# Kernel tuning notes

Measured on AMD Instinct MI355X. Metric: run time of the kernel, lower is better.

The kernel has to match this reference:

```python
import jax, jax.numpy as jnp
import numpy as np

B, N, F, T = 64, 1024, 8, 12
H, NLAYERS, K, OUT = 32, 3, 10, 12
E_RAND = N * 32


def setup_inputs() -> dict:
    key = jax.random.key(0)
    ks = jax.random.split(key, 11)
    x = jax.random.normal(ks[0], (B, N, F, T), jnp.float32)
    src = jax.random.randint(ks[1], (E_RAND,), 0, N)
    dst = jax.random.randint(ks[2], (E_RAND,), 0, N)
    loop = jnp.arange(N)
    edge_index = jnp.stack([jnp.concatenate([src, loop]),
                            jnp.concatenate([dst, loop])]).astype(jnp.int32)
    # weights in (0.1, 1.0) so all degrees are strictly positive
    edge_weight = jax.random.uniform(ks[3], (E_RAND + N,), jnp.float32, 0.1, 1.0)
    s = 0.1  # ~ 1/sqrt(H) init scale, matches torch defaults in spirit
    gru_w_ih = jax.random.normal(ks[4], (3 * H, F), jnp.float32) * s
    gru_w_hh = jax.random.normal(ks[5], (3 * H, H), jnp.float32) * s
    gru_b_ih = jax.random.normal(ks[6], (3 * H,), jnp.float32) * s
    gru_b_hh = jax.random.normal(ks[7], (3 * H,), jnp.float32) * s
    conv_w = jax.random.normal(ks[8], (NLAYERS, H, H), jnp.float32) * (1.0 / np.sqrt(H))
    lin_w = jax.random.normal(ks[9], (H, OUT), jnp.float32) * (1.0 / np.sqrt(H))
    lin_b = jax.random.normal(ks[10], (OUT,), jnp.float32) * s
    return {"x": x, "edge_index": edge_index, "edge_weight": edge_weight,
            "gru_w_ih": gru_w_ih, "gru_w_hh": gru_w_hh,
            "gru_b_ih": gru_b_ih, "gru_b_hh": gru_b_hh,
            "conv_w": conv_w, "lin_w": lin_w, "lin_b": lin_b}


def reference(x, edge_index, edge_weight, gru_w_ih, gru_w_hh, gru_b_ih, gru_b_hh,
              conv_w, lin_w, lin_b):
    Bsz, Nn, Fe, Tt = x.shape
    Hh = gru_w_hh.shape[1]

    # ---- temporal GRU over [B*N, T, F], keep last hidden state ----
    xt = jnp.transpose(x, (0, 1, 3, 2)).reshape(Bsz * Nn, Tt, Fe)
    gates_x = xt @ gru_w_ih.T + gru_b_ih  # [BN, T, 3H], input gates precomputed

    def step(h, gx):
        gh = h @ gru_w_hh.T + gru_b_hh
        xr, xz, xn = jnp.split(gx, 3, axis=-1)
        hr, hz, hn = jnp.split(gh, 3, axis=-1)
        r = jax.nn.sigmoid(xr + hr)
        z = jax.nn.sigmoid(xz + hz)
        n = jnp.tanh(xn + r * hn)
        return (1.0 - z) * n + z * h, None

    h0 = jnp.zeros((Bsz * Nn, Hh), x.dtype)
    hT, _ = jax.lax.scan(step, h0, jnp.swapaxes(gates_x, 0, 1))
    h = hT.reshape(Bsz, Nn, Hh)  # [B, N, H]

    # ---- normalized Laplacian (shared across batch) ----
    A = jnp.zeros((Nn, Nn), x.dtype).at[edge_index[0], edge_index[1]].add(edge_weight)
    d_isqrt = 1.0 / jnp.sqrt(A.sum(axis=1))  # row-degree, matches A.sum(dim=2)
    Lap = jnp.eye(Nn, dtype=x.dtype) - d_isqrt[:, None] * A * d_isqrt[None, :]

    # ---- rank-K spectral filter: M = U_k diag(S_k) U_k^T ----
    # torch code SVDs the identical L[b] per batch element; sign flips of U
    # columns cancel in U_k (.) U_k^T, so one SVD is mathematically identical.
    U, S, _ = jnp.linalg.svd(Lap, full_matrices=False)
    M = (U[:, :K] * S[:K]) @ U[:, :K].T  # [N, N]

    for w in conv_w:  # static 3-layer loop
        h = jax.nn.relu(jnp.einsum('nm,bmh,hk->bnk', M, h, w)) + h

    return h @ lin_w + lin_b  # [B, N, 12]
```

## Files before the change

kernel.cpp:

```cpp
#include <hip/hip_runtime.h>
#include <math.h>


#define NN 1024
#define PP 48
#define JSWEEPS 3
#define NROUNDS (JSWEEPS * (PP - 1))

typedef float v2f __attribute__((ext_vector_type(2)));

__global__ __launch_bounds__(256) void k_gru(
    const float* __restrict__ x, const float* __restrict__ wih,
    const float* __restrict__ whh, const float* __restrict__ bih,
    const float* __restrict__ bhh, float* __restrict__ hout) {
  __shared__ float s_x[64][97];
  __shared__ float s_h[64][33];
  int tid = threadIdx.x;
  int row = tid & 63;
  int i_base = __builtin_amdgcn_readfirstlane((tid >> 6) * 8);
  long row0 = (long)blockIdx.x * 64;

  for (int i = tid; i < 64 * 24; i += 256) {
    int r = i / 24, c = i % 24;
    float4 v = *(const float4*)&x[(row0 + r) * 96 + c * 4];
    s_x[r][c * 4 + 0] = v.x; s_x[r][c * 4 + 1] = v.y;
    s_x[r][c * 4 + 2] = v.z; s_x[r][c * 4 + 3] = v.w;
  }
  for (int i = tid; i < 64 * 32; i += 256) s_h[i / 32][i % 32] = 0.f;
  __syncthreads();

  v2f h2[16];
#pragma unroll
  for (int k2 = 0; k2 < 16; ++k2) h2[k2] = (v2f){0.f, 0.f};

  for (int t = 0; t < 12; ++t) {
    v2f x2[4];
#pragma unroll
    for (int f2 = 0; f2 < 4; ++f2)
      x2[f2] = (v2f){s_x[row][(2 * f2) * 12 + t], s_x[row][(2 * f2 + 1) * 12 + t]};
    for (int ii = 0; ii < 8; ++ii) {
      int i = i_base + ii;
      const v2f* wr = (const v2f*)(wih + i * 8);
      const v2f* wz = (const v2f*)(wih + (32 + i) * 8);
      const v2f* wn = (const v2f*)(wih + (64 + i) * 8);
      const v2f* hr = (const v2f*)(whh + i * 32);
      const v2f* hz = (const v2f*)(whh + (32 + i) * 32);
      const v2f* hn = (const v2f*)(whh + (64 + i) * 32);
      v2f ar2 = (v2f){0.f, 0.f}, az2 = (v2f){0.f, 0.f};
      v2f gx2 = (v2f){0.f, 0.f}, gh2 = (v2f){0.f, 0.f};
#pragma unroll
      for (int f2 = 0; f2 < 4; ++f2) {
        ar2 += x2[f2] * wr[f2];
        az2 += x2[f2] * wz[f2];
        gx2 += x2[f2] * wn[f2];
      }
#pragma unroll
      for (int k2 = 0; k2 < 16; ++k2) {
        ar2 += h2[k2] * hr[k2];
        az2 += h2[k2] * hz[k2];
        gh2 += h2[k2] * hn[k2];
      }
      float ar = ar2.x + ar2.y + bih[i] + bhh[i];
      float az = az2.x + az2.y + bih[32 + i] + bhh[32 + i];
      float gx = gx2.x + gx2.y + bih[64 + i];
      float gh = gh2.x + gh2.y + bhh[64 + i];
      ar = fminf(fmaxf(ar, -30.f), 30.f);
      az = fminf(fmaxf(az, -30.f), 30.f);
      float r = __frcp_rn(1.f + __expf(-ar));
      float z = __frcp_rn(1.f + __expf(-az));
      float a = gx + r * gh;
      a = fminf(fmaxf(a, -15.f), 15.f);
      float e2 = __expf(2.f * a);
      float n = (e2 - 1.f) * __frcp_rn(e2 + 1.f);
      float hold = s_h[row][i];
      s_h[row][i] = (1.f - z) * n + z * hold;
    }
    __syncthreads();
#pragma unroll
    for (int k2 = 0; k2 < 16; ++k2)
      h2[k2] = (v2f){s_h[row][2 * k2], s_h[row][2 * k2 + 1]};
    __syncthreads();
  }
  for (int idx = tid; idx < 64 * 8; idx += 256) {
    int r = idx >> 3, c4 = idx & 7;
    float4 v = make_float4(s_h[r][c4 * 4], s_h[r][c4 * 4 + 1],
                           s_h[r][c4 * 4 + 2], s_h[r][c4 * 4 + 3]);
    *(float4*)&hout[(row0 + r) * 32 + c4 * 4] = v;
  }
}

__global__ void k_scatter(const int* __restrict__ ei, const float* __restrict__ ew,
                          float* __restrict__ A, int E) {
  int e = blockIdx.x * 256 + threadIdx.x;
  if (e < E) atomicAdd(&A[ei[e] * NN + ei[E + e]], ew[e]);
}

__global__ __launch_bounds__(256) void k_degree(const float* __restrict__ A,
                                                float* __restrict__ disq) {
  __shared__ float red[256];
  int row = blockIdx.x, tid = threadIdx.x;
  float s = 0.f;
  for (int j = tid; j < NN; j += 256) s += A[row * NN + j];
  red[tid] = s;
  __syncthreads();
  for (int off = 128; off > 0; off >>= 1) {
    if (tid < off) red[tid] += red[tid + off];
    __syncthreads();
  }
  if (tid == 0) disq[row] = 1.f / sqrtf(red[0]);
}

template <int LAP>
__global__ __launch_bounds__(256) void k_mmsplit(const float* __restrict__ A,
                                                 const float* __restrict__ disq,
                                                 float* __restrict__ Cp) {
  __shared__ float As[32][68];
  __shared__ float Bs[32][68];
  int tid = threadIdx.x;
  int tx = tid & 15, ty = tid >> 4;
  int i0 = blockIdx.y * 64, j0 = blockIdx.x * 64;
  int kbase = blockIdx.z * 512;
  v2f acc2[4][2];
#pragma unroll
  for (int a = 0; a < 4; ++a) {
    acc2[a][0] = (v2f){0.f, 0.f};
    acc2[a][1] = (v2f){0.f, 0.f};
  }
  int lrow = tid >> 3;
  int kk0 = (tid & 7) * 4;
  float drA0 = 0.f, drA1 = 0.f, drB0 = 0.f, drB1 = 0.f;
  if (LAP) {
    drA0 = disq[i0 + lrow]; drA1 = disq[i0 + lrow + 32];
    drB0 = disq[j0 + lrow]; drB1 = disq[j0 + lrow + 32];
  }
  float4 pa0 = *(const float4*)&A[(long)(i0 + lrow) * NN + kbase + kk0];
  float4 pa1 = *(const float4*)&A[(long)(i0 + lrow + 32) * NN + kbase + kk0];
  float4 pb0 = *(const float4*)&A[(long)(j0 + lrow) * NN + kbase + kk0];
  float4 pb1 = *(const float4*)&A[(long)(j0 + lrow + 32) * NN + kbase + kk0];
  for (int k0 = kbase; k0 < kbase + 512; k0 += 32) {
    if (LAP) {
      float4 dq = *(const float4*)&disq[k0 + kk0];
      int kg = k0 + kk0;
#pragma unroll
      for (int e = 0; e < 4; ++e) {
        float dqe = (e == 0) ? dq.x : (e == 1) ? dq.y : (e == 2) ? dq.z : dq.w;
        float a0e = (e == 0) ? pa0.x : (e == 1) ? pa0.y : (e == 2) ? pa0.z : pa0.w;
        float a1e = (e == 0) ? pa1.x : (e == 1) ? pa1.y : (e == 2) ? pa1.z : pa1.w;
        float b0e = (e == 0) ? pb0.x : (e == 1) ? pb0.y : (e == 2) ? pb0.z : pb0.w;
        float b1e = (e == 0) ? pb1.x : (e == 1) ? pb1.y : (e == 2) ? pb1.z : pb1.w;
        As[kk0 + e][lrow]      = -drA0 * a0e * dqe + ((i0 + lrow == kg + e) ? 1.f : 0.f);
        As[kk0 + e][lrow + 32] = -drA1 * a1e * dqe + ((i0 + lrow + 32 == kg + e) ? 1.f : 0.f);
        Bs[kk0 + e][lrow]      = -drB0 * b0e * dqe + ((j0 + lrow == kg + e) ? 1.f : 0.f);
        Bs[kk0 + e][lrow + 32] = -drB1 * b1e * dqe + ((j0 + lrow + 32 == kg + e) ? 1.f : 0.f);
      }
    } else {
      As[kk0 + 0][lrow] = pa0.x; As[kk0 + 1][lrow] = pa0.y;
      As[kk0 + 2][lrow] = pa0.z; As[kk0 + 3][lrow] = pa0.w;
      As[kk0 + 0][lrow + 32] = pa1.x; As[kk0 + 1][lrow + 32] = pa1.y;
      As[kk0 + 2][lrow + 32] = pa1.z; As[kk0 + 3][lrow + 32] = pa1.w;
      Bs[kk0 + 0][lrow] = pb0.x; Bs[kk0 + 1][lrow] = pb0.y;
      Bs[kk0 + 2][lrow] = pb0.z; Bs[kk0 + 3][lrow] = pb0.w;
      Bs[kk0 + 0][lrow + 32] = pb1.x; Bs[kk0 + 1][lrow + 32] = pb1.y;
      Bs[kk0 + 2][lrow + 32] = pb1.z; Bs[kk0 + 3][lrow + 32] = pb1.w;
    }
    __syncthreads();
    if (k0 + 32 < kbase + 512) {
      pa0 = *(const float4*)&A[(long)(i0 + lrow) * NN + k0 + 32 + kk0];
      pa1 = *(const float4*)&A[(long)(i0 + lrow + 32) * NN + k0 + 32 + kk0];
      pb0 = *(const float4*)&A[(long)(j0 + lrow) * NN + k0 + 32 + kk0];
      pb1 = *(const float4*)&A[(long)(j0 + lrow + 32) * NN + k0 + 32 + kk0];
    }
#pragma unroll
    for (int kk = 0; kk < 32; ++kk) {
      float4 av = *(const float4*)&As[kk][ty * 4];
      const v2f* bp = (const v2f*)&Bs[kk][tx * 4];
      v2f bv0 = bp[0], bv1 = bp[1];
      float aa[4] = {av.x, av.y, av.z, av.w};
#pragma unroll
      for (int a = 0; a < 4; ++a) {
        v2f ab = (v2f){aa[a], aa[a]};
        acc2[a][0] += ab * bv0;
        acc2[a][1] += ab * bv1;
      }
    }
    __syncthreads();
  }
  float* cp = Cp + (long)blockIdx.z * (NN * NN);
#pragma unroll
  for (int a = 0; a < 4; ++a) {
    float4 v = make_float4(acc2[a][0].x, acc2[a][0].y,
                           acc2[a][1].x, acc2[a][1].y);
    *(float4*)&cp[(long)(i0 + ty * 4 + a) * NN + j0 + tx * 4] = v;
  }
}

__global__ __launch_bounds__(256) void k_fold(const float* __restrict__ Cp,
                                              float* __restrict__ C) {
  int i = (blockIdx.x * 256 + threadIdx.x) * 4;
  float4 a = *(const float4*)&Cp[i];
  float4 b = *(const float4*)&Cp[i + NN * NN];
  float4 v = make_float4(a.x + b.x, a.y + b.y, a.z + b.z, a.w + b.w);
  *(float4*)&C[i] = v;
}

__global__ void k_q0(float* __restrict__ Q) {
  int i = blockIdx.x * 256 + threadIdx.x;
  if (i < NN * PP) {
    unsigned u = (unsigned)i * 2654435761u;
    u ^= u >> 16; u *= 2246822519u; u ^= u >> 13; u *= 3266489917u; u ^= u >> 16;
    Q[i] = (float)(u & 0xFFFFFF) * (1.f / 16777216.f) - 0.5f;
  }
}

__global__ __launch_bounds__(256) void k_spmm(const float* __restrict__ Gp,
                                              const float* __restrict__ Q,
                                              float* __restrict__ Zp) {
  __shared__ float Qs[64][49];
  __shared__ float Gs[16][65];
  int tid = threadIdx.x;
  int r = tid >> 4;
  int c0 = (tid & 15) * 3;
  int row0 = blockIdx.x * 16;
  int k0 = blockIdx.y * 256;
  float a0 = 0.f, a1 = 0.f, a2 = 0.f;
  for (int kt = 0; kt < 4; ++kt) {
    int kb = k0 + kt * 64;
    for (int idx = tid; idx < 64 * PP; idx += 256) {
      int qr = idx / PP, qc = idx % PP;
      Qs[qr][qc] = Q[(kb + qr) * PP + qc];
    }
    for (int idx = tid; idx < 16 * 64; idx += 256) {
      int gr = idx >> 6, gk = idx & 63;
      Gs[gr][gk] = Gp[(long)(row0 + gr) * NN + kb + gk];
    }
    __syncthreads();
#pragma unroll 4
    for (int kk = 0; kk < 64; ++kk) {
      float g = Gs[r][kk];
      a0 += g * Qs[kk][c0];
      a1 += g * Qs[kk][c0 + 1];
      a2 += g * Qs[kk][c0 + 2];
    }
    __syncthreads();
  }
  float* zp = Zp + (long)blockIdx.y * (NN * PP);
  zp[(row0 + r) * PP + c0] = a0;
  zp[(row0 + r) * PP + c0 + 1] = a1;
  zp[(row0 + r) * PP + c0 + 2] = a2;
}

__global__ __launch_bounds__(256) void k_gram(const float* __restrict__ Zp,
                                              float* __restrict__ Z,
                                              float* __restrict__ Sp) {
  __shared__ float Zs[32][49];
  int tid = threadIdx.x;
  int r0 = blockIdx.x * 32;
  for (int idx = tid; idx < 32 * PP; idx += 256) {
    int r = idx / PP, c = idx % PP;
    long g = (long)(r0 + r) * PP + c;
    float s = Zp[g] + Zp[g + NN * PP] + Zp[g + 2 * NN * PP] + Zp[g + 3 * NN * PP];
    Zs[r][c] = s;
    Z[g] = s;
  }
  __syncthreads();
  float* sp = Sp + blockIdx.x * (PP * PP);
  for (int cell = tid; cell < PP * PP; cell += 256) {
    int i = cell / PP, j = cell % PP;
    float a = 0.f;
#pragma unroll 8
    for (int r = 0; r < 32; ++r) a += Zs[r][i] * Zs[r][j];
    sp[cell] = a;
  }
}

__global__ __launch_bounds__(256) void k_tbuild(const float* __restrict__ Qa,
                                                const float* __restrict__ Zp,
                                                float* __restrict__ Tp) {
  __shared__ float Qs[32][49];
  __shared__ float Ys[32][49];
  int tid = threadIdx.x;
  int r0 = blockIdx.x * 32;
  for (int idx = tid; idx < 32 * PP; idx += 256) {
    int r = idx / PP, c = idx % PP;
    long g = (long)(r0 + r) * PP + c;
    Qs[r][c] = Qa[g];
    Ys[r][c] = Zp[g] + Zp[g + NN * PP] + Zp[g + 2 * NN * PP] + Zp[g + 3 * NN * PP];
  }
  __syncthreads();
  float* tp = Tp + blockIdx.x * (PP * PP);
  for (int cell = tid; cell < PP * PP; cell += 256) {
    int i = cell / PP, j = cell % PP;
    float a = 0.f;
#pragma unroll 8
    for (int r = 0; r < 32; ++r) a += Qs[r][i] * Ys[r][j];
    tp[cell] = a;
  }
}

__global__ __launch_bounds__(256) void k_qr(const float* __restrict__ Sp,
                                            float* __restrict__ Q) {
  __shared__ float R[PP][PP + 1];
  __shared__ float rs[PP];
  __shared__ float idiag[PP];
  int tid = threadIdx.x;
  for (int idx = tid; idx < PP * PP; idx += 256) {
    float s = 0.f;
    for (int b = 0; b < 32; ++b) s += Sp[b * (PP * PP) + idx];
    R[idx / PP][idx % PP] = s;
  }
  __syncthreads();
  for (int j = 0; j < PP; ++j) {
    float d = R[j][j];
    float sq = sqrtf(d > 1e-30f ? d : 1e-30f);
    float invd = 1.f / sq;
    for (int c = j + tid; c < PP; c += 256)
      rs[c] = (c == j) ? sq : R[j][c] * invd;
    __syncthreads();
    int m = PP - 1 - j;
    for (int idx = tid; idx < m * m; idx += 256) {
      int i = j + 1 + idx / m, c = j + 1 + idx % m;
      R[i][c] -= rs[i] * rs[c];
    }
    for (int c = j + tid; c < PP; c += 256) R[j][c] = rs[c];
    __syncthreads();
  }
  if (tid < PP) idiag[tid] = 1.f / R[tid][tid];
  __syncthreads();
  int row = blockIdx.x * 256 + tid;
  float q[PP];
#pragma unroll
  for (int k = 0; k < PP; ++k) q[k] = Q[row * PP + k];
#pragma unroll
  for (int c = 0; c < PP; ++c) {
    float s = q[c];
#pragma unroll
    for (int k = 0; k < c; ++k) s -= q[k] * R[k][c];
    q[c] = s * idiag[c];
  }
#pragma unroll
  for (int k = 0; k < PP; ++k) Q[row * PP + k] = q[k];
}

__global__ __launch_bounds__(448) void k_jacobi(const float* __restrict__ Tp,
                                                float* __restrict__ Vsel,
                                                float* __restrict__ s10) {
  __shared__ float Ta[PP][PP + 1], Tb[PP][PP + 1];
  __shared__ float Va[PP][PP + 1], Vb[PP][PP + 1];
  __shared__ float cw0[2][PP], cw1[2][PP];
  __shared__ int ci0[2][PP], ci1[2][PP];
  __shared__ int ppair[2][24], qpair[2][24];
  __shared__ float cpair[2][24], spair[2][24];
  __shared__ int selidx[10];
  int tid = threadIdx.x;
  for (int idx = tid; idx < PP * PP; idx += 448) {
    float s = 0.f;
    for (int b = 0; b < 32; ++b) s += Tp[b * (PP * PP) + idx];
    Tb[idx / PP][idx % PP] = s;
  }
  __syncthreads();
  for (int idx = tid; idx < PP * PP; idx += 448) {
    int i = idx / PP, j = idx % PP;
    Ta[i][j] = 0.5f * (Tb[i][j] + Tb[j][i]);
    Va[i][j] = (i == j) ? 1.f : 0.f;
  }
  if (tid < PP) {
    ci0[0][tid] = tid; ci1[0][tid] = tid;
    cw0[0][tid] = 1.f; cw1[0][tid] = 0.f;
  }
  __syncthreads();
  float (*Tc)[PP + 1] = Ta, (*Tn)[PP + 1] = Tb;
  float (*Vc)[PP + 1] = Va, (*Vn)[PP + 1] = Vb;

  auto coeff_phase = [&](int rr, int cur, int nxt, float (*Tcur)[PP + 1]) {
    int k = tid - 384;
    int P = (k == 0) ? 0 : ((rr + k - 1) % 47) + 1;
    int Q = ((rr + 46 - k) % 47) + 1;
    int P0 = ci0[cur][P], P1 = ci1[cur][P];
    float Pw0 = cw0[cur][P], Pw1 = cw1[cur][P];
    int Q0 = ci0[cur][Q], Q1 = ci1[cur][Q];
    float Qw0 = cw0[cur][Q], Qw1 = cw1[cur][Q];
    float app = Pw0 * (Pw0 * Tcur[P0][P0] + Pw1 * Tcur[P0][P1]) +
                Pw1 * (Pw0 * Tcur[P1][P0] + Pw1 * Tcur[P1][P1]);
    float apq = Pw0 * (Qw0 * Tcur[P0][Q0] + Qw1 * Tcur[P0][Q1]) +
                Pw1 * (Qw0 * Tcur[P1][Q0] + Qw1 * Tcur[P1][Q1]);
    float aqq = Qw0 * (Qw0 * Tcur[Q0][Q0] + Qw1 * Tcur[Q0][Q1]) +
                Qw1 * (Qw0 * Tcur[Q1][Q0] + Qw1 * Tcur[Q1][Q1]);
    float c = 1.f, s = 0.f;
    if (fabsf(apq) > 1e-30f) {
      float tau = (aqq - app) / (2.f * apq);
      float den = fabsf(tau) + sqrtf(1.f + tau * tau);
      float tt = copysignf(1.f / den, tau);
      c = 1.f / sqrtf(1.f + tt * tt);
      s = tt * c;
    }
    ci0[nxt][P] = P; ci1[nxt][P] = Q; cw0[nxt][P] = c;  cw1[nxt][P] = -s;
    ci0[nxt][Q] = P; ci1[nxt][Q] = Q; cw0[nxt][Q] = s;  cw1[nxt][Q] = c;
    ppair[nxt][k] = P; qpair[nxt][k] = Q;
    cpair[nxt][k] = c; spair[nxt][k] = s;
  };

  if (tid >= 384 && tid < 408) coeff_phase(0, 0, 1, Tc);
  __syncthreads();

  int cur = 1;
  int i_row = tid >> 3;
  int kb = (tid & 7) * 3;
  for (int R = 0; R < NROUNDS; ++R) {
    if (tid < 384) {
      float wi0 = cw0[cur][i_row], wi1 = cw1[cur][i_row];
      int i0 = ci0[cur][i_row], i1 = ci1[cur][i_row];
#pragma unroll
      for (int m = 0; m < 3; ++m) {
        int k = kb + m;
        int p = ppair[cur][k], q = qpair[cur][k];
        float c = cpair[cur][k], s = spair[cur][k];
        float t00 = Tc[i0][p], t01 = Tc[i0][q];
        float t10 = Tc[i1][p], t11 = Tc[i1][q];
        float rp = wi0 * t00 + wi1 * t10;
        float rq = wi0 * t01 + wi1 * t11;
        Tn[i_row][p] = c * rp - s * rq;
        Tn[i_row][q] = s * rp + c * rq;
        float v0 = Vc[i_row][p], v1 = Vc[i_row][q];
        Vn[i_row][p] = c * v0 - s * v1;
        Vn[i_row][q] = s * v0 + c * v1;
      }
    } else if (tid < 408 && R + 1 < NROUNDS) {
      coeff_phase((R + 1) % 47, cur, cur ^ 1, Tc);
    }
    __syncthreads();
    float (*tt_)[PP + 1] = Tc; Tc = Tn; Tn = tt_;
    float (*vt_)[PP + 1] = Vc; Vc = Vn; Vn = vt_;
    cur ^= 1;
  }

  if (tid < 64) {
    float v = (tid < PP) ? Tc[tid][tid] : -1e30f;
    for (int sel = 0; sel < 10; ++sel) {
      float bv = v; int bi = tid;
      for (int off = 32; off > 0; off >>= 1) {
        float ov = __shfl_xor(bv, off);
        int oi = __shfl_xor(bi, off);
        if (ov > bv || (ov == bv && oi < bi)) { bv = ov; bi = oi; }
      }
      if (tid == 0) { selidx[sel] = bi; s10[sel] = sqrtf(fmaxf(bv, 0.f)); }
      if (tid == bi) v = -1e30f;
    }
  }
  __syncthreads();
  for (int idx = tid; idx < PP * 10; idx += 448) {
    int j = idx / 10, i = idx % 10;
    Vsel[idx] = Vc[j][selidx[i]];
  }
}

__global__ __launch_bounds__(256) void k_u10(const float* __restrict__ Q,
                                             const float* __restrict__ Vsel,
                                             float* __restrict__ U10) {
  __shared__ float Vs[PP * 10];
  int tid = threadIdx.x;
  for (int idx = tid; idx < PP * 10; idx += 256) Vs[idx] = Vsel[idx];
  __syncthreads();
  int row = blockIdx.x * 256 + tid;
  float q[PP];
#pragma unroll
  for (int k = 0; k < PP; ++k) q[k] = Q[row * PP + k];
#pragma unroll
  for (int i = 0; i < 10; ++i) {
    float s = 0.f;
#pragma unroll
    for (int k = 0; k < PP; ++k) s += q[k] * Vs[k * 10 + i];
    U10[row * 10 + i] = s;
  }
}

__global__ __launch_bounds__(320) void k_p0(const float* __restrict__ h,
                                            const float* __restrict__ U10,
                                            float* __restrict__ Pp) {
  __shared__ float Hs[128][33];
  __shared__ float Us[128][10];
  int tid = threadIdx.x;
  int b = blockIdx.x >> 2, ch = blockIdx.x & 3;
  int i = tid / 32, kk = tid % 32;
  int base = ch * 256;
  v2f acc2 = (v2f){0.f, 0.f};
  for (int t0 = 0; t0 < 256; t0 += 128) {
    for (int idx = tid; idx < 128 * 32; idx += 320) {
      int r = idx / 32, c = idx % 32;
      Hs[r][c] = h[(long)(b * NN + base + t0 + r) * 32 + c];
    }
    for (int idx = tid; idx < 1280; idx += 320)
      Us[idx / 10][idx % 10] = U10[(base + t0 + idx / 10) * 10 + idx % 10];
    __syncthreads();
#pragma unroll 8
    for (int r = 0; r < 128; r += 2) {
      acc2 += (v2f){Us[r][i], Us[r + 1][i]} * (v2f){Hs[r][kk], Hs[r + 1][kk]};
    }
    __syncthreads();
  }
  Pp[(long)blockIdx.x * 320 + tid] = acc2.x + acc2.y;
}

template <int LAST>
__global__ __launch_bounds__(256) void k_update(float* __restrict__ h,
                                                const float* __restrict__ U10,
                                                const float* __restrict__ Pp,
                                                const float* __restrict__ W,
                                                const float* __restrict__ s10,
                                                const float* __restrict__ lw,
                                                const float* __restrict__ lb,
                                                float* __restrict__ out) {
  __shared__ float P0s[10][32];
  __shared__ float P1s[10][32];
  __shared__ float Ws[32][32];
  __shared__ float Us[64][10];
  __shared__ float hl[64][33];
  int tid = threadIdx.x;
  int b = blockIdx.x, n0 = blockIdx.y * 64;
  for (int idx = tid; idx < 320; idx += 256) {
    long g = (long)b * 4 * 320 + idx;
    P0s[idx / 32][idx % 32] = Pp[g] + Pp[g + 320] + Pp[g + 640] + Pp[g + 960];
  }
  for (int idx = tid; idx < 1024; idx += 256) Ws[idx / 32][idx % 32] = W[idx];
  for (int idx = tid; idx < 640; idx += 256)
    Us[idx / 10][idx % 10] = U10[(n0 + idx / 10) * 10 + idx % 10];
  __syncthreads();
  for (int idx = tid; idx < 320; idx += 256) {
    int i = idx / 32, kk = idx % 32;
    float a = 0.f;
#pragma unroll
    for (int j = 0; j < 32; ++j) a += P0s[i][j] * Ws[j][kk];
    P1s[i][kk] = s10[i] * a;
  }
  __syncthreads();
  for (int idx = tid; idx < 2048; idx += 256) {
    int nl = idx / 32, k = idx % 32;
    float z = 0.f;
#pragma unroll
    for (int i = 0; i < 10; ++i) z += Us[nl][i] * P1s[i][k];
    long g = (long)(b * NN + n0 + nl) * 32 + k;
    float hn = h[g] + fmaxf(z, 0.f);
    if (LAST) hl[nl][k] = hn;
    else h[g] = hn;
  }
  if (LAST) {
    __syncthreads();
    for (int idx = tid; idx < 64 * 12; idx += 256) {
      int row = idx / 12, o = idx % 12;
      float s = lb[o];
#pragma unroll
      for (int j = 0; j < 32; ++j) s += hl[row][j] * lw[j * 12 + o];
      out[(long)(b * NN + n0 + row) * 12 + o] = s;
    }
  }
}

extern "C" void kernel_launch(void* const* d_in, const int* in_sizes, int n_in,
                              void* d_out, int out_size, void* d_ws, size_t ws_size,
                              hipStream_t stream) {
  const float* x    = (const float*)d_in[0];
  const int*   ei   = (const int*)d_in[1];
  const float* ew   = (const float*)d_in[2];
  const float* wih  = (const float*)d_in[3];
  const float* whh  = (const float*)d_in[4];
  const float* bih  = (const float*)d_in[5];
  const float* bhh  = (const float*)d_in[6];
  const float* convw = (const float*)d_in[7];
  const float* lw   = (const float*)d_in[8];
  const float* lb   = (const float*)d_in[9];
  float* out = (float*)d_out;
  float* ws  = (float*)d_ws;
  int E = in_sizes[1] / 2;

  float* h    = ws;
  float* B1   = h + 2097152;
  float* B2   = B1 + 1048576;
  float* B3   = B2 + 1048576;
  float* Qa   = B3 + 1048576;
  float* Qb   = Qa + 49152;
  float* Zp   = Qb + 49152;
  float* Sp   = Zp + 196608;
  float* Tp   = Sp + 73728;
  float* Vsel = Tp + 73728;
  float* s10  = Vsel + 480;
  float* U10  = s10 + 16;
  float* disq = U10 + 10240;
  float* Pp   = Zp;
  float* Cp   = h;

  hipMemsetAsync(B1, 0, (size_t)1048576 * 4, stream);
  k_scatter<<<(E + 255) / 256, 256, 0, stream>>>(ei, ew, B1, E);
  k_degree<<<NN, 256, 0, stream>>>(B1, disq);
  k_mmsplit<1><<<dim3(16, 16, 2), 256, 0, stream>>>(B1, disq, Cp);
  k_fold<<<1024, 256, 0, stream>>>(Cp, B2);
  k_mmsplit<0><<<dim3(16, 16, 2), 256, 0, stream>>>(B2, disq, Cp);
  k_fold<<<1024, 256, 0, stream>>>(Cp, B3);
  k_mmsplit<0><<<dim3(16, 16, 2), 256, 0, stream>>>(B3, disq, Cp);
  k_fold<<<1024, 256, 0, stream>>>(Cp, B1);
  k_mmsplit<0><<<dim3(16, 16, 2), 256, 0, stream>>>(B1, disq, Cp);
  k_fold<<<1024, 256, 0, stream>>>(Cp, B3);
  k_mmsplit<0><<<dim3(16, 16, 2), 256, 0, stream>>>(B3, disq, Cp);
  k_fold<<<1024, 256, 0, stream>>>(Cp, B1);
  k_mmsplit<0><<<dim3(16, 16, 2), 256, 0, stream>>>(B1, disq, Cp);
  k_fold<<<1024, 256, 0, stream>>>(Cp, B3);

  k_q0<<<192, 256, 0, stream>>>(Qa);
  for (int it = 0; it < 6; ++it) {
    float* src = (it & 1) ? Qb : Qa;
    float* dst = (it & 1) ? Qa : Qb;
    k_spmm<<<dim3(64, 4), 256, 0, stream>>>(B3, src, Zp);
    k_gram<<<32, 256, 0, stream>>>(Zp, dst, Sp);
    k_qr<<<4, 256, 0, stream>>>(Sp, dst);
  }

  k_spmm<<<dim3(64, 4), 256, 0, stream>>>(B2, Qa, Zp);
  k_tbuild<<<32, 256, 0, stream>>>(Qa, Zp, Tp);
  k_jacobi<<<1, 448, 0, stream>>>(Tp, Vsel, s10);
  k_u10<<<4, 256, 0, stream>>>(Qa, Vsel, U10);

  k_gru<<<1024, 256, 0, stream>>>(x, wih, whh, bih, bhh, h);

  for (int l = 0; l < 3; ++l) {
    k_p0<<<256, 320, 0, stream>>>(h, U10, Pp);
    if (l < 2)
      k_update<0><<<dim3(64, 16), 256, 0, stream>>>(h, U10, Pp, convw + l * 1024,
                                                    s10, lw, lb, out);
    else
      k_update<1><<<dim3(64, 16), 256, 0, stream>>>(h, U10, Pp, convw + l * 1024,
                                                    s10, lw, lb, out);
  }
}
```

Before: 1.073 ms.

## Retile Gram-power matmuls to 128x128 blocks with 4-way split-K

Replaces the 64x64-tile, 2-way split-K matmul with a 128x128-tile kernel where each thread computes an 8x8 output block over 16-deep K slices, using 4-way split-K. The aim is higher register-level reuse and fewer LDS reads per FMA in the six repeated-squaring matmuls. To hold the extra partial sums, buffers are reassigned and a new B4 buffer is added, and the fold kernel now sums four partials instead of two. The cost is more fold traffic, higher register pressure and a larger workspace. Grid size drops from 512 to 256 blocks.

```diff
diff --git a/kernel.cpp b/kernel.cpp
--- a/kernel.cpp
+++ b/kernel.cpp
@@ -111,95 +111,98 @@
 }
 
 template <int LAP>
-__global__ __launch_bounds__(256) void k_mmsplit(const float* __restrict__ A,
-                                                 const float* __restrict__ disq,
-                                                 float* __restrict__ Cp) {
-  __shared__ float As[32][68];
-  __shared__ float Bs[32][68];
+__global__ __launch_bounds__(256) void k_mm128(const float* __restrict__ A,
+                                               const float* __restrict__ disq,
+                                               float* __restrict__ Cp0,
+                                               float* __restrict__ Cp2,
+                                               float* __restrict__ Cp3) {
+  __shared__ float As[16][132];
+  __shared__ float Bs[16][132];
   int tid = threadIdx.x;
   int tx = tid & 15, ty = tid >> 4;
-  int i0 = blockIdx.y * 64, j0 = blockIdx.x * 64;
-  int kbase = blockIdx.z * 512;
-  v2f acc2[4][2];
-#pragma unroll
-  for (int a = 0; a < 4; ++a) {
-    acc2[a][0] = (v2f){0.f, 0.f};
-    acc2[a][1] = (v2f){0.f, 0.f};
-  }
-  int lrow = tid >> 3;
-  int kk0 = (tid & 7) * 4;
-  float drA0 = 0.f, drA1 = 0.f, drB0 = 0.f, drB1 = 0.f;
-  if (LAP) {
-    drA0 = disq[i0 + lrow]; drA1 = disq[i0 + lrow + 32];
-    drB0 = disq[j0 + lrow]; drB1 = disq[j0 + lrow + 32];
-  }
-  float4 pa0 = *(const float4*)&A[(long)(i0 + lrow) * NN + kbase + kk0];
-  float4 pa1 = *(const float4*)&A[(long)(i0 + lrow + 32) * NN + kbase + kk0];
-  float4 pb0 = *(const float4*)&A[(long)(j0 + lrow) * NN + kbase + kk0];
-  float4 pb1 = *(const float4*)&A[(long)(j0 + lrow + 32) * NN + kbase + kk0];
-  for (int k0 = kbase; k0 < kbase + 512; k0 += 32) {
+  int i0 = blockIdx.y * 128, j0 = blockIdx.x * 128;
+  int kbase = blockIdx.z * 256;
+  v2f acc2[8][4];
+#pragma unroll
+  for (int r = 0; r < 8; ++r)
+#pragma unroll
+    for (int c = 0; c < 4; ++c) acc2[r][c] = (v2f){0.f, 0.f};
+  int lrow = tid >> 1;
+  int koff = (tid & 1) * 8;
+  float dA = 0.f, dB = 0.f;
+  if (LAP) { dA = disq[i0 + lrow]; dB = disq[j0 + lrow]; }
+  float4 pa0 = *(const float4*)&A[(long)(i0 + lrow) * NN + kbase + koff];
+  float4 pa1 = *(const float4*)&A[(long)(i0 + lrow) * NN + kbase + koff + 4];
+  float4 pb0 = *(const float4*)&A[(long)(j0 + lrow) * NN + kbase + koff];
+  float4 pb1 = *(const float4*)&A[(long)(j0 + lrow) * NN + kbase + koff + 4];
+  for (int k0 = kbase; k0 < kbase + 256; k0 += 16) {
+    float pa[8] = {pa0.x, pa0.y, pa0.z, pa0.w, pa1.x, pa1.y, pa1.z, pa1.w};
+    float pb[8] = {pb0.x, pb0.y, pb0.z, pb0.w, pb1.x, pb1.y, pb1.z, pb1.w};
     if (LAP) {
-      float4 dq = *(const float4*)&disq[k0 + kk0];
-      int kg = k0 + kk0;
-#pragma unroll
-      for (int e = 0; e < 4; ++e) {
-        float dqe = (e == 0) ? dq.x : (e == 1) ? dq.y : (e == 2) ? dq.z : dq.w;
-        float a0e = (e == 0) ? pa0.x : (e == 1) ? pa0.y : (e == 2) ? pa0.z : pa0.w;
-        float a1e = (e == 0) ? pa1.x : (e == 1) ? pa1.y : (e == 2) ? pa1.z : pa1.w;
-        float b0e = (e == 0) ? pb0.x : (e == 1) ? pb0.y : (e == 2) ? pb0.z : pb0.w;
-        float b1e = (e == 0) ? pb1.x : (e == 1) ? pb1.y : (e == 2) ? pb1.z : pb1.w;
-        As[kk0 + e][lrow]      = -drA0 * a0e * dqe + ((i0 + lrow == kg + e) ? 1.f : 0.f);
-        As[kk0 + e][lrow + 32] = -drA1 * a1e * dqe + ((i0 + lrow + 32 == kg + e) ? 1.f : 0.f);
-        Bs[kk0 + e][lrow]      = -drB0 * b0e * dqe + ((j0 + lrow == kg + e) ? 1.f : 0.f);
-        Bs[kk0 + e][lrow + 32] = -drB1 * b1e * dqe + ((j0 + lrow + 32 == kg + e) ? 1.f : 0.f);
+      float4 dq0 = *(const float4*)&disq[k0 + koff];
+      float4 dq1 = *(const float4*)&disq[k0 + koff + 4];
+      float dq[8] = {dq0.x, dq0.y, dq0.z, dq0.w, dq1.x, dq1.y, dq1.z, dq1.w};
+#pragma unroll
+      for (int e = 0; e < 8; ++e) {
+        int kg = k0 + koff + e;
+        As[koff + e][lrow] = -dA * pa[e] * dq[e] + ((i0 + lrow == kg) ? 1.f : 0.f);
+        Bs[koff + e][lrow] = -dB * pb[e] * dq[e] + ((j0 + lrow == kg) ? 1.f : 0.f);
       }
     } else {
-      As[kk0 + 0][lrow] = pa0.x; As[kk0 + 1][lrow] = pa0.y;
-      As[kk0 + 2][lrow] = pa0.z; As[kk0 + 3][lrow] = pa0.w;
-      As[kk0 + 0][lrow + 32] = pa1.x; As[kk0 + 1][lrow + 32] = pa1.y;
-      As[kk0 + 2][lrow + 32] = pa1.z; As[kk0 + 3][lrow + 32] = pa1.w;
-      Bs[kk0 + 0][lrow] = pb0.x; Bs[kk0 + 1][lrow] = pb0.y;
-      Bs[kk0 + 2][lrow] = pb0.z; Bs[kk0 + 3][lrow] = pb0.w;
-      Bs[kk0 + 0][lrow + 32] = pb1.x; Bs[kk0 + 1][lrow + 32] = pb1.y;
-      Bs[kk0 + 2][lrow + 32] = pb1.z; Bs[kk0 + 3][lrow + 32] = pb1.w;
-    }
-    __syncthreads();
-    if (k0 + 32 < kbase + 512) {
-      pa0 = *(const float4*)&A[(long)(i0 + lrow) * NN + k0 + 32 + kk0];
-      pa1 = *(const float4*)&A[(long)(i0 + lrow + 32) * NN + k0 + 32 + kk0];
-      pb0 = *(const float4*)&A[(long)(j0 + lrow) * NN + k0 + 32 + kk0];
-      pb1 = *(const float4*)&A[(long)(j0 + lrow + 32) * NN + k0 + 32 + kk0];
-    }
-#pragma unroll
-    for (int kk = 0; kk < 32; ++kk) {
-      float4 av = *(const float4*)&As[kk][ty * 4];
-      const v2f* bp = (const v2f*)&Bs[kk][tx * 4];
-      v2f bv0 = bp[0], bv1 = bp[1];
-      float aa[4] = {av.x, av.y, av.z, av.w};
-#pragma unroll
-      for (int a = 0; a < 4; ++a) {
-        v2f ab = (v2f){aa[a], aa[a]};
-        acc2[a][0] += ab * bv0;
-        acc2[a][1] += ab * bv1;
+#pragma unroll
+      for (int e = 0; e < 8; ++e) {
+        As[koff + e][lrow] = pa[e];
+        Bs[koff + e][lrow] = pb[e];
       }
     }
     __syncthreads();
-  }
-  float* cp = Cp + (long)blockIdx.z * (NN * NN);
-#pragma unroll
-  for (int a = 0; a < 4; ++a) {
-    float4 v = make_float4(acc2[a][0].x, acc2[a][0].y,
-                           acc2[a][1].x, acc2[a][1].y);
-    *(float4*)&cp[(long)(i0 + ty * 4 + a) * NN + j0 + tx * 4] = v;
-  }
-}
-
-__global__ __launch_bounds__(256) void k_fold(const float* __restrict__ Cp,
+    if (k0 + 16 < kbase + 256) {
+      pa0 = *(const float4*)&A[(long)(i0 + lrow) * NN + k0 + 16 + koff];
+      pa1 = *(const float4*)&A[(long)(i0 + lrow) * NN + k0 + 16 + koff + 4];
+      pb0 = *(const float4*)&A[(long)(j0 + lrow) * NN + k0 + 16 + koff];
+      pb1 = *(const float4*)&A[(long)(j0 + lrow) * NN + k0 + 16 + koff + 4];
+    }
+#pragma unroll
+    for (int kk = 0; kk < 16; ++kk) {
+      float4 a0 = *(const float4*)&As[kk][ty * 8];
+      float4 a1 = *(const float4*)&As[kk][ty * 8 + 4];
+      float4 b0 = *(const float4*)&Bs[kk][tx * 8];
+      float4 b1 = *(const float4*)&Bs[kk][tx * 8 + 4];
+      v2f bv[4] = {(v2f){b0.x, b0.y}, (v2f){b0.z, b0.w},
+                   (v2f){b1.x, b1.y}, (v2f){b1.z, b1.w}};
+      float aa[8] = {a0.x, a0.y, a0.z, a0.w, a1.x, a1.y, a1.z, a1.w};
+#pragma unroll
+      for (int r = 0; r < 8; ++r) {
+        v2f ar = (v2f){aa[r], aa[r]};
+#pragma unroll
+        for (int c = 0; c < 4; ++c) acc2[r][c] += ar * bv[c];
+      }
+    }
+    __syncthreads();
+  }
+  float* cp = (blockIdx.z < 2) ? (Cp0 + (long)blockIdx.z * (NN * NN))
+                               : (blockIdx.z == 2 ? Cp2 : Cp3);
+#pragma unroll
+  for (int r = 0; r < 8; ++r) {
+    long row = i0 + ty * 8 + r;
+    *(float4*)&cp[row * NN + j0 + tx * 8] =
+        make_float4(acc2[r][0].x, acc2[r][0].y, acc2[r][1].x, acc2[r][1].y);
+    *(float4*)&cp[row * NN + j0 + tx * 8 + 4] =
+        make_float4(acc2[r][2].x, acc2[r][2].y, acc2[r][3].x, acc2[r][3].y);
+  }
+}
+
+__global__ __launch_bounds__(256) void k_fold(const float* __restrict__ Cp0,
+                                              const float* __restrict__ Cp2,
+                                              const float* __restrict__ Cp3,
                                               float* __restrict__ C) {
   int i = (blockIdx.x * 256 + threadIdx.x) * 4;
-  float4 a = *(const float4*)&Cp[i];
-  float4 b = *(const float4*)&Cp[i + NN * NN];
-  float4 v = make_float4(a.x + b.x, a.y + b.y, a.z + b.z, a.w + b.w);
+  float4 a = *(const float4*)&Cp0[i];
+  float4 b = *(const float4*)&Cp0[i + NN * NN];
+  float4 c = *(const float4*)&Cp2[i];
+  float4 d = *(const float4*)&Cp3[i];
+  float4 v = make_float4(a.x + b.x + c.x + d.x, a.y + b.y + c.y + d.y,
+                         a.z + b.z + c.z + d.z, a.w + b.w + c.w + d.w);
   *(float4*)&C[i] = v;
 }
 
@@ -575,7 +578,8 @@
   float* B1   = h + 2097152;
   float* B2   = B1 + 1048576;
   float* B3   = B2 + 1048576;
-  float* Qa   = B3 + 1048576;
+  float* B4   = B3 + 1048576;
+  float* Qa   = B4 + 1048576;
   float* Qb   = Qa + 49152;
   float* Zp   = Qb + 49152;
   float* Sp   = Zp + 196608;
@@ -585,34 +589,35 @@
   float* U10  = s10 + 16;
   float* disq = U10 + 10240;
   float* Pp   = Zp;
-  float* Cp   = h;
 
   hipMemsetAsync(B1, 0, (size_t)1048576 * 4, stream);
   k_scatter<<<(E + 255) / 256, 256, 0, stream>>>(ei, ew, B1, E);
   k_degree<<<NN, 256, 0, stream>>>(B1, disq);
-  k_mmsplit<1><<<dim3(16, 16, 2), 256, 0, stream>>>(B1, disq, Cp);
-  k_fold<<<1024, 256, 0, stream>>>(Cp, B2);
-  k_mmsplit<0><<<dim3(16, 16, 2), 256, 0, stream>>>(B2, disq, Cp);
-  k_fold<<<1024, 256, 0, stream>>>(Cp, B3);
-  k_mmsplit<0><<<dim3(16, 16, 2), 256, 0, stream>>>(B3, disq, Cp);
-  k_fold<<<1024, 256, 0, stream>>>(Cp, B1);
-  k_mmsplit<0><<<dim3(16, 16, 2), 256, 0, stream>>>(B1, disq, Cp);
-  k_fold<<<1024, 256, 0, stream>>>(Cp, B3);
-  k_mmsplit<0><<<dim3(16, 16, 2), 256, 0, stream>>>(B3, disq, Cp);
-  k_fold<<<1024, 256, 0, stream>>>(Cp, B1);
-  k_mmsplit<0><<<dim3(16, 16, 2), 256, 0, stream>>>(B1, disq, Cp);
-  k_fold<<<1024, 256, 0, stream>>>(Cp, B3);
+  k_mm128<1><<<dim3(8, 8, 4), 256, 0, stream>>>(B1, disq, h, B2, B3);
+  k_fold<<<1024, 256, 0, stream>>>(h, B2, B3, B4);
+  k_mm128<0><<<dim3(8, 8, 4), 256, 0, stream>>>(B4, disq, h, B2, B3);
+  k_fold<<<1024, 256, 0, stream>>>(h, B2, B3, B1);
+  k_mm128<0><<<dim3(8, 8, 4), 256, 0, stream>>>(B1, disq, h, B2, B3);
+  k_fold<<<1024, 256, 0, stream>>>(h, B2, B3, B3);
+  k_mm128<0><<<dim3(8, 8, 4), 256, 0, stream>>>(B3, disq, h, B2, B1);
+  k_fold<<<1024, 256, 0, stream>>>(h, B2, B1, B1);
+  k_mm128<0><<<dim3(8, 8, 4), 256, 0, stream>>>(B1, disq, h, B2, B3);
+  k_fold<<<1024, 256, 0, stream>>>(h, B2, B3, B3);
+  k_mm128<0><<<dim3(8, 8, 4), 256, 0, stream>>>(B3, disq, h, B2, B1);
+  k_fold<<<1024, 256, 0, stream>>>(h, B2, B1, B1);
+  float* G32 = B1;
+  float* G   = B4;
 
   k_q0<<<192, 256, 0, stream>>>(Qa);
   for (int it = 0; it < 6; ++it) {
     float* src = (it & 1) ? Qb : Qa;
     float* dst = (it & 1) ? Qa : Qb;
-    k_spmm<<<dim3(64, 4), 256, 0, stream>>>(B3, src, Zp);
+    k_spmm<<<dim3(64, 4), 256, 0, stream>>>(G32, src, Zp);
     k_gram<<<32, 256, 0, stream>>>(Zp, dst, Sp);
     k_qr<<<4, 256, 0, stream>>>(Sp, dst);
   }
 
-  k_spmm<<<dim3(64, 4), 256, 0, stream>>>(B2, Qa, Zp);
+  k_spmm<<<dim3(64, 4), 256, 0, stream>>>(G, Qa, Zp);
   k_tbuild<<<32, 256, 0, stream>>>(Qa, Zp, Tp);
   k_jacobi<<<1, 448, 0, stream>>>(Tp, Vsel, s10);
   k_u10<<<4, 256, 0, stream>>>(Qa, Vsel, U10);
```

Result: no change. 1.083 ms (+1.0%).
